# Optimization experiments

Measured on AMD Instinct MI355X. Metric: run time of the kernel, lower is better.

The kernel has to match this reference:

```python
import jax, jax.numpy as jnp
import numpy as np
from jax import lax

DN = ('NCHW', 'OIHW', 'NCHW')


def _conv(x, w, pad):
    return lax.conv_general_dilated(x, w, (1, 1), [(pad, pad), (pad, pad)], dimension_numbers=DN)


def _bn(x, gamma, beta, mean, var, eps=1e-5):
    inv = gamma * lax.rsqrt(var + eps)
    return x * inv[None, :, None, None] + (beta - mean * inv)[None, :, None, None]


def _unfold(x, K, pad):
    # torch.nn.Unfold layout: channel-major, kernel positions fastest -> (B, C, K*K, H, W)
    B, C, H, W = x.shape
    p = lax.conv_general_dilated_patches(x, (K, K), (1, 1), [(pad, pad), (pad, pad)], dimension_numbers=DN)
    return p.reshape(B, C, K * K, H, W)


def setup_inputs() -> dict:
    key = jax.random.key(0)
    ks = jax.random.split(key, 16)
    B, C, H, W, K = 16, 64, 64, 64, 3
    d = {
        'x': jax.random.normal(ks[0], (B, C, H, W), jnp.float32),
        'wq': jax.random.normal(ks[1], (C, C, 1, 1), jnp.float32) * 0.1,
        'wk': jax.random.normal(ks[2], (C, C, K, K), jnp.float32) * 0.05,
        'wv': jax.random.normal(ks[3], (C, C, 1, 1), jnp.float32) * 0.1,
        'pos_h': jax.random.normal(ks[4], (C, K, 1), jnp.float32),
        'pos_w': jax.random.normal(ks[5], (C, 1, K), jnp.float32),
    }
    for i, nm in enumerate(['q', 'k', 'v', 'o']):
        d[nm + '_gamma'] = jnp.ones((C,), jnp.float32)
        d[nm + '_beta'] = jnp.zeros((C,), jnp.float32)
        d[nm + '_mean'] = jax.random.normal(ks[6 + i], (C,), jnp.float32) * 0.1
        d[nm + '_var'] = jax.random.uniform(ks[10 + i], (C,), jnp.float32, 0.5, 1.5)
    return d


def reference(x, wq, q_gamma, q_beta, q_mean, q_var,
              wk, k_gamma, k_beta, k_mean, k_var,
              wv, v_gamma, v_beta, v_mean, v_var,
              pos_h, pos_w, o_gamma, o_beta, o_mean, o_var):
    B, C, H, W = x.shape
    K = pos_h.shape[1]
    heads = C // 8
    cph = C // heads  # channels per head

    q = jax.nn.relu(_bn(_conv(x, wq, 0), q_gamma, q_beta, q_mean, q_var))
    k = jax.nn.relu(_bn(_conv(x, wk, K // 2), k_gamma, k_beta, k_mean, k_var))
    v = _bn(_conv(x, wv, 0), v_gamma, v_beta, v_mean, v_var)

    # local keys + positional bias: (B, C, K*K, H, W)
    unfold_k = _unfold(k, K, K // 2)
    pos = (pos_h + pos_w).reshape(1, C, K * K, 1, 1)
    kp = (unfold_k + pos).reshape(B, heads, cph, K * K, H, W)
    qh = q.reshape(B, heads, cph, 1, H, W)

    attn = (qh * kp).sum(axis=2)            # (B, heads, K*K, H, W)
    attn = jax.nn.softmax(attn, axis=2)

    # local aggregation (LocalConvolution): weights shared across cph channels per head
    uv = _unfold(v, K, (K - 1) // 2).reshape(B, heads, cph, K * K, H, W)
    out = (attn[:, :, None] * uv).sum(axis=3).reshape(B, C, H, W)

    out = jax.nn.relu(_bn(out, o_gamma, o_beta, o_mean, o_var))
    return out
```

## Files before the change

kernel.cpp:

```cpp
#include <hip/hip_runtime.h>
#include <hip/hip_bf16.h>
#include <math.h>

#define B_ 16
#define C_ 64
#define H_ 64
#define W_ 64
#define KSTEPS 18

typedef __attribute__((ext_vector_type(8))) short bf16x8;
typedef __attribute__((ext_vector_type(4))) short bf16x4;
typedef __attribute__((ext_vector_type(4))) float f32x4;

static __device__ __forceinline__ unsigned short f2b(float f) {
    __hip_bfloat16 h = __float2bfloat16(f);
    return *reinterpret_cast<unsigned short*>(&h);
}
static __device__ __forceinline__ float b2f(unsigned short u) {
    __hip_bfloat16 h;
    *reinterpret_cast<unsigned short*>(&h) = u;
    return __bfloat162float(h);
}

__global__ __launch_bounds__(64) void prep_kernel(
    const float* __restrict__ wq, const float* __restrict__ wk, const float* __restrict__ wv,
    const float* __restrict__ qg, const float* __restrict__ qb, const float* __restrict__ qm, const float* __restrict__ qv,
    const float* __restrict__ kg, const float* __restrict__ kb, const float* __restrict__ km, const float* __restrict__ kv,
    const float* __restrict__ vg, const float* __restrict__ vb, const float* __restrict__ vm, const float* __restrict__ vv,
    const float* __restrict__ og, const float* __restrict__ ob, const float* __restrict__ om, const float* __restrict__ ov,
    unsigned short* __restrict__ Wp, float* __restrict__ bnp)
{
    const int bid = blockIdx.x;
    const int lane = threadIdx.x;
    if (bid < 12 * KSTEPS) {
        const int mf = bid / KSTEPS;
        const int ks = bid % KSTEPS;
        const int r = lane & 15;
        bf16x8 u;
#pragma unroll
        for (int j = 0; j < 8; j++) {
            int k = ks * 32 + ((lane >> 4) << 3) + j;
            int tap = k >> 6;
            int c = k & 63;
            float w;
            if (mf < 4)      { int co = mf * 16 + r;        w = (tap == 4) ? wq[co * 64 + c] : 0.f; }
            else if (mf < 8) { int co = (mf - 4) * 16 + r;  w = wk[(co * 64 + c) * 9 + tap]; }
            else             { int co = (mf - 8) * 16 + r;  w = (tap == 4) ? wv[co * 64 + c] : 0.f; }
            u[j] = (short)f2b(w);
        }
        *reinterpret_cast<bf16x8*>(Wp + ((size_t)(mf * KSTEPS + ks) * 64 + lane) * 8) = u;
    } else {
        const int c = lane;
        const float* G[4] = {qg, kg, vg, og};
        const float* Bt[4] = {qb, kb, vb, ob};
        const float* M[4] = {qm, km, vm, om};
        const float* V[4] = {qv, kv, vv, ov};
#pragma unroll
        for (int p = 0; p < 4; p++) {
            float inv = G[p][c] * rsqrtf(V[p][c] + 1e-5f);
            bnp[p * 128 + c] = inv;
            bnp[p * 128 + 64 + c] = Bt[p][c] - M[p][c] * inv;
        }
    }
}

__global__ __launch_bounds__(512) void qkv_mfma2(
    const float* __restrict__ x, const unsigned short* __restrict__ Wp,
    const float* __restrict__ bnp,
    unsigned short* __restrict__ qt, unsigned short* __restrict__ kt, unsigned short* __restrict__ vt)
{
    __shared__ __align__(16) char xs[4 * 66 * 64 * 2];
    __shared__ float bns[384];
    const int bid = blockIdx.x;
    const int b  = bid >> 5;
    const int h0 = (bid & 31) << 1;
    const int tid = threadIdx.x;

    for (int i = tid; i < 4 * 66 * 8; i += 512) {
        int col = i % 66;
        int dy  = (i / 66) & 3;
        int c0g = i / 264;
        int gh = h0 - 1 + dy, gw = col - 1;
        bool ok = ((unsigned)gh < 64u) && ((unsigned)gw < 64u);
        bf16x8 u;
#pragma unroll
        for (int j = 0; j < 8; j++) {
            float f = ok ? x[((b * 64 + c0g * 8 + j) * 64 + gh) * 64 + gw] : 0.f;
            u[j] = (short)f2b(f);
        }
        int La = ((dy * 66 + col) * 64 + c0g * 8) * 2;
        La ^= (col & 7) << 4;
        *reinterpret_cast<bf16x8*>(xs + La) = u;
    }
    if (tid < 384) bns[tid] = bnp[tid];
    __syncthreads();

    const int wid = tid >> 6, lane = tid & 63;
    const int mfg = wid >> 1, nfg = wid & 1;
    const int t = lane & 15, q4 = lane >> 4;

    f32x4 acc[3][4];
#pragma unroll
    for (int m = 0; m < 3; m++)
#pragma unroll
        for (int n = 0; n < 4; n++) acc[m][n] = (f32x4){0.f, 0.f, 0.f, 0.f};

    for (int ks = 0; ks < KSTEPS; ks++) {
        const int tap = ks >> 1;
        const int dy = tap / 3, dx = tap - dy * 3;
        const int kb = (ks & 1) * 32 + q4 * 8;
        bf16x8 bf[4];
#pragma unroll
        for (int n = 0; n < 4; n++) {
            int p = (nfg * 4 + n) * 16 + t;
            int r = p >> 6, colw = p & 63;
            int col = colw + dx;
            int La = (((r + dy) * 66 + col) * 64 + kb) * 2;
            La ^= (col & 7) << 4;
            bf[n] = *reinterpret_cast<const bf16x8*>(xs + La);
        }
#pragma unroll
        for (int m = 0; m < 3; m++) {
            int mf = mfg * 3 + m;
            bf16x8 af = *reinterpret_cast<const bf16x8*>(Wp + ((size_t)(mf * KSTEPS + ks) * 64 + lane) * 8);
#pragma unroll
            for (int n = 0; n < 4; n++)
                acc[m][n] = __builtin_amdgcn_mfma_f32_16x16x32_bf16(af, bf[n], acc[m][n], 0, 0, 0);
        }
    }

#pragma unroll
    for (int m = 0; m < 3; m++) {
        int mf = mfg * 3 + m;
        int plane = mf >> 2;
        int co0 = mf * 16 + q4 * 4;
        int c0 = co0 & 63;
        f32x4 inv  = *reinterpret_cast<const f32x4*>(&bns[plane * 128 + c0]);
        f32x4 bias = *reinterpret_cast<const f32x4*>(&bns[plane * 128 + 64 + c0]);
        unsigned short* base = (plane == 0 ? qt : plane == 1 ? kt : vt);
#pragma unroll
        for (int n = 0; n < 4; n++) {
            int p = (nfg * 4 + n) * 16 + t;
            int r = p >> 6, colw = p & 63;
            bf16x4 pack;
#pragma unroll
            for (int j = 0; j < 4; j++) {
                float val = acc[m][n][j] * inv[j] + bias[j];
                if (plane < 2) val = fmaxf(val, 0.f);
                pack[j] = (short)f2b(val);
            }
            *reinterpret_cast<bf16x4*>(base + ((size_t)((b * 64 + h0 + r) * 64 + colw)) * 64 + c0) = pack;
        }
    }
}

__global__ __launch_bounds__(512) void attn3_kernel(
    const unsigned short* __restrict__ qt, const unsigned short* __restrict__ kt,
    const unsigned short* __restrict__ vt,
    const float* __restrict__ ph, const float* __restrict__ pw,
    const float* __restrict__ bnp, float* __restrict__ out)
{
    __shared__ __align__(16) char ksm[3 * 66 * 64 * 2];
    __shared__ __align__(16) char vsm[3 * 66 * 64 * 2];
    __shared__ float bno[128];
    const int bid = blockIdx.x;
    const int b = bid >> 6;
    const int h = bid & 63;
    const int tid = threadIdx.x;

    for (int i = tid; i < 3 * 66 * 8; i += 512) {
        int c8  = i & 7;
        int pxp = (i >> 3) % 66;
        int dy  = (i >> 3) / 66;
        int gh = h + dy - 1, gw = pxp - 1;
        bool ok = ((unsigned)gh < 64u) && ((unsigned)gw < 64u);
        int La = ((dy * 66 + pxp) * 64 + c8 * 8) * 2;
        La ^= (pxp & 7) << 4;
        bf16x8 kk = (bf16x8){0,0,0,0,0,0,0,0}, vv = kk;
        if (ok) {
            size_t src = ((size_t)((b * 64 + gh) * 64 + gw)) * 64 + c8 * 8;
            kk = *reinterpret_cast<const bf16x8*>(kt + src);
            vv = *reinterpret_cast<const bf16x8*>(vt + src);
        }
        *reinterpret_cast<bf16x8*>(ksm + La) = kk;
        *reinterpret_cast<bf16x8*>(vsm + La) = vv;
    }
    if (tid < 128) bno[tid] = bnp[384 + tid];
    __syncthreads();

    const int px = tid & 63;
    const int head = tid >> 6;
    const int cb = head * 8;

    float qf[8];
    {
        bf16x8 q8 = *reinterpret_cast<const bf16x8*>(qt + ((size_t)((b * 64 + h) * 64 + px)) * 64 + cb);
#pragma unroll
        for (int j = 0; j < 8; j++) qf[j] = b2f((unsigned short)q8[j]);
    }

    float A[3], Bx[3];
#pragma unroll
    for (int tt = 0; tt < 3; tt++) {
        float a = 0.f, bb = 0.f;
#pragma unroll
        for (int j = 0; j < 8; j++) {
            a  = fmaf(qf[j], ph[(cb + j) * 3 + tt], a);
            bb = fmaf(qf[j], pw[(cb + j) * 3 + tt], bb);
        }
        A[tt] = a; Bx[tt] = bb;
    }

    float logit[9];
#pragma unroll
    for (int dy = 0; dy < 3; dy++) {
#pragma unroll
        for (int dx = 0; dx < 3; dx++) {
            int pxp = px + dx;
            int La = ((dy * 66 + pxp) * 64 + cb) * 2;
            La ^= (pxp & 7) << 4;
            bf16x8 k8 = *reinterpret_cast<const bf16x8*>(ksm + La);
            float qk = 0.f;
#pragma unroll
            for (int j = 0; j < 8; j++) qk = fmaf(qf[j], b2f((unsigned short)k8[j]), qk);
            logit[dy * 3 + dx] = qk + A[dy] + Bx[dx];
        }
    }

    float m = logit[0];
#pragma unroll
    for (int tt = 1; tt < 9; tt++) m = fmaxf(m, logit[tt]);
    float e[9], sum = 0.f;
#pragma unroll
    for (int tt = 0; tt < 9; tt++) { e[tt] = __expf(logit[tt] - m); sum += e[tt]; }
    float inv = 1.f / sum;

    float o[8];
#pragma unroll
    for (int j = 0; j < 8; j++) o[j] = 0.f;
#pragma unroll
    for (int dy = 0; dy < 3; dy++) {
#pragma unroll
        for (int dx = 0; dx < 3; dx++) {
            int pxp = px + dx;
            int La = ((dy * 66 + pxp) * 64 + cb) * 2;
            La ^= (pxp & 7) << 4;
            bf16x8 v8 = *reinterpret_cast<const bf16x8*>(vsm + La);
            float w = e[dy * 3 + dx];
#pragma unroll
            for (int j = 0; j < 8; j++) o[j] = fmaf(w, b2f((unsigned short)v8[j]), o[j]);
        }
    }

#pragma unroll
    for (int j = 0; j < 8; j++) {
        int c = cb + j;
        float val = fmaxf(fmaf(o[j] * inv, bno[c], bno[64 + c]), 0.f);
        out[((size_t)(b * C_ + c) * H_ + h) * W_ + px] = val;
    }
}

extern "C" void kernel_launch(void* const* d_in, const int* in_sizes, int n_in,
                              void* d_out, int out_size, void* d_ws, size_t ws_size,
                              hipStream_t stream)
{
    const float* x   = (const float*)d_in[0];
    const float* wq  = (const float*)d_in[1];
    const float* wk  = (const float*)d_in[2];
    const float* wv  = (const float*)d_in[3];
    const float* ph  = (const float*)d_in[4];
    const float* pw  = (const float*)d_in[5];
    const float* qg  = (const float*)d_in[6];
    const float* qb  = (const float*)d_in[7];
    const float* qm  = (const float*)d_in[8];
    const float* qv  = (const float*)d_in[9];
    const float* kg  = (const float*)d_in[10];
    const float* kb  = (const float*)d_in[11];
    const float* km  = (const float*)d_in[12];
    const float* kv  = (const float*)d_in[13];
    const float* vg  = (const float*)d_in[14];
    const float* vb  = (const float*)d_in[15];
    const float* vm  = (const float*)d_in[16];
    const float* vv  = (const float*)d_in[17];
    const float* og  = (const float*)d_in[18];
    const float* ob  = (const float*)d_in[19];
    const float* om  = (const float*)d_in[20];
    const float* ov  = (const float*)d_in[21];

    char* ws = (char*)d_ws;
    unsigned short* Wp = (unsigned short*)ws;
    float* bnp = (float*)(ws + 221184);
    unsigned short* qt = (unsigned short*)(ws + 223232);
    unsigned short* kt = qt + (size_t)B_ * H_ * W_ * C_;
    unsigned short* vt = kt + (size_t)B_ * H_ * W_ * C_;

    prep_kernel<<<12 * KSTEPS + 1, 64, 0, stream>>>(
        wq, wk, wv, qg, qb, qm, qv, kg, kb, km, kv, vg, vb, vm, vv,
        og, ob, om, ov, Wp, bnp);

    qkv_mfma2<<<B_ * H_ / 2, 512, 0, stream>>>(x, Wp, bnp, qt, kt, vt);

    attn3_kernel<<<B_ * H_, 512, 0, stream>>>(qt, kt, vt, ph, pw, bnp, (float*)d_out);
}
```

Measured before the change: 156.3 us.

## Fuse QKV convolution with local attention, recomputing halo rows in shared memory

The QKV MFMA convolution and the attention kernel are merged into one kernel per output row. Each block computes Q, K and V for a 3-row neighborhood (recomputing halo rows that neighbouring blocks also compute) and keeps them in LDS, so the bf16 q/k/v tensors are no longer written to and re-read from global memory. A separate transpose kernel first converts x to a channel-last bf16 layout so the fused kernel can load its 5-row input halo with vector loads. The trade-off is about 1.5x redundant convolution MFMA work, more accumulator registers, and larger LDS use per block.

Result: no change. 157.3 us (+0.6%).

```diff
diff --git a/kernel.cpp b/kernel.cpp
--- a/kernel.cpp
+++ b/kernel.cpp
@@ -64,83 +64,109 @@
     }
 }
 
-__global__ __launch_bounds__(512) void qkv_mfma2(
-    const float* __restrict__ x, const unsigned short* __restrict__ Wp,
+__global__ __launch_bounds__(256) void xt_kernel(
+    const float* __restrict__ x, unsigned short* __restrict__ xt)
+{
+    __shared__ float ls[64][65];
+    const int b = blockIdx.x >> 6;
+    const int h = blockIdx.x & 63;
+    const int tid = threadIdx.x;
+    const int w = tid & 63;
+    const int cg = tid >> 6;
+#pragma unroll
+    for (int cc = 0; cc < 16; cc++) {
+        int c = cg * 16 + cc;
+        ls[c][w] = x[((b * 64 + c) * 64 + h) * 64 + w];
+    }
+    __syncthreads();
+    const int px = tid & 63;
+    bf16x8 u0, u1;
+#pragma unroll
+    for (int j = 0; j < 8; j++) {
+        u0[j] = (short)f2b(ls[cg * 16 + j][px]);
+        u1[j] = (short)f2b(ls[cg * 16 + 8 + j][px]);
+    }
+    size_t base = ((size_t)((b * 64 + h) * 64 + px)) * 64 + cg * 16;
+    *reinterpret_cast<bf16x8*>(xt + base) = u0;
+    *reinterpret_cast<bf16x8*>(xt + base + 8) = u1;
+}
+
+#define KSM_OFF 0
+#define VSM_OFF 25344
+#define QSM_OFF 50688
+__global__ __launch_bounds__(512, 4) void fused_kernel(
+    const unsigned short* __restrict__ xt, const unsigned short* __restrict__ Wp,
     const float* __restrict__ bnp,
-    unsigned short* __restrict__ qt, unsigned short* __restrict__ kt, unsigned short* __restrict__ vt)
+    const float* __restrict__ ph, const float* __restrict__ pw,
+    float* __restrict__ out)
 {
-    __shared__ __align__(16) char xs[4 * 66 * 64 * 2];
-    __shared__ float bns[384];
+    __shared__ __align__(16) char smem[58880];
+    __shared__ float bns[512];
     const int bid = blockIdx.x;
-    const int b  = bid >> 5;
-    const int h0 = (bid & 31) << 1;
+    const int b = bid >> 6;
+    const int h = bid & 63;
     const int tid = threadIdx.x;
 
-    for (int i = tid; i < 4 * 66 * 8; i += 512) {
-        int col = i % 66;
-        int dy  = (i / 66) & 3;
-        int c0g = i / 264;
-        int gh = h0 - 1 + dy, gw = col - 1;
-        bool ok = ((unsigned)gh < 64u) && ((unsigned)gw < 64u);
-        bf16x8 u;
-#pragma unroll
-        for (int j = 0; j < 8; j++) {
-            float f = ok ? x[((b * 64 + c0g * 8 + j) * 64 + gh) * 64 + gw] : 0.f;
-            u[j] = (short)f2b(f);
-        }
-        int La = ((dy * 66 + col) * 64 + c0g * 8) * 2;
+    for (int i = tid; i < 5 * 66 * 8; i += 512) {
+        int ch  = i & 7;
+        int col = (i >> 3) % 66;
+        int dy  = (i >> 3) / 66;
+        int gh = h - 2 + dy, gw = col - 1;
+        bf16x8 u = (bf16x8){0,0,0,0,0,0,0,0};
+        if ((unsigned)gh < 64u && (unsigned)gw < 64u)
+            u = *reinterpret_cast<const bf16x8*>(xt + ((size_t)((b * 64 + gh) * 64 + gw)) * 64 + ch * 8);
+        int La = ((dy * 66 + col) * 64 + ch * 8) * 2;
         La ^= (col & 7) << 4;
-        *reinterpret_cast<bf16x8*>(xs + La) = u;
-    }
-    if (tid < 384) bns[tid] = bnp[tid];
+        *reinterpret_cast<bf16x8*>(smem + La) = u;
+    }
+    bns[tid < 512 ? tid : 0] = bnp[tid < 512 ? tid : 0];
     __syncthreads();
 
     const int wid = tid >> 6, lane = tid & 63;
     const int mfg = wid >> 1, nfg = wid & 1;
     const int t = lane & 15, q4 = lane >> 4;
 
-    f32x4 acc[3][4];
+    f32x4 acc[3][6];
 #pragma unroll
     for (int m = 0; m < 3; m++)
 #pragma unroll
-        for (int n = 0; n < 4; n++) acc[m][n] = (f32x4){0.f, 0.f, 0.f, 0.f};
+        for (int n = 0; n < 6; n++) acc[m][n] = (f32x4){0.f, 0.f, 0.f, 0.f};
 
     for (int ks = 0; ks < KSTEPS; ks++) {
         const int tap = ks >> 1;
         const int dy = tap / 3, dx = tap - dy * 3;
         const int kb = (ks & 1) * 32 + q4 * 8;
-        bf16x8 bf[4];
-#pragma unroll
-        for (int n = 0; n < 4; n++) {
-            int p = (nfg * 4 + n) * 16 + t;
+        bf16x8 bf[6];
+#pragma unroll
+        for (int n = 0; n < 6; n++) {
+            int p = (nfg * 6 + n) * 16 + t;
             int r = p >> 6, colw = p & 63;
             int col = colw + dx;
             int La = (((r + dy) * 66 + col) * 64 + kb) * 2;
             La ^= (col & 7) << 4;
-            bf[n] = *reinterpret_cast<const bf16x8*>(xs + La);
+            bf[n] = *reinterpret_cast<const bf16x8*>(smem + La);
         }
 #pragma unroll
         for (int m = 0; m < 3; m++) {
             int mf = mfg * 3 + m;
             bf16x8 af = *reinterpret_cast<const bf16x8*>(Wp + ((size_t)(mf * KSTEPS + ks) * 64 + lane) * 8);
 #pragma unroll
-            for (int n = 0; n < 4; n++)
+            for (int n = 0; n < 6; n++)
                 acc[m][n] = __builtin_amdgcn_mfma_f32_16x16x32_bf16(af, bf[n], acc[m][n], 0, 0, 0);
         }
     }
+    __syncthreads();
 
 #pragma unroll
     for (int m = 0; m < 3; m++) {
         int mf = mfg * 3 + m;
         int plane = mf >> 2;
-        int co0 = mf * 16 + q4 * 4;
-        int c0 = co0 & 63;
+        int c0 = (mf * 16 + q4 * 4) & 63;
         f32x4 inv  = *reinterpret_cast<const f32x4*>(&bns[plane * 128 + c0]);
         f32x4 bias = *reinterpret_cast<const f32x4*>(&bns[plane * 128 + 64 + c0]);
-        unsigned short* base = (plane == 0 ? qt : plane == 1 ? kt : vt);
-#pragma unroll
-        for (int n = 0; n < 4; n++) {
-            int p = (nfg * 4 + n) * 16 + t;
+#pragma unroll
+        for (int n = 0; n < 6; n++) {
+            int p = (nfg * 6 + n) * 16 + t;
             int r = p >> 6, colw = p & 63;
             bf16x4 pack;
 #pragma unroll
@@ -149,43 +175,46 @@
                 if (plane < 2) val = fmaxf(val, 0.f);
                 pack[j] = (short)f2b(val);
             }
-            *reinterpret_cast<bf16x4*>(base + ((size_t)((b * 64 + h0 + r) * 64 + colw)) * 64 + c0) = pack;
-        }
-    }
-}
-
-__global__ __launch_bounds__(512) void attn3_kernel(
-    const unsigned short* __restrict__ qt, const unsigned short* __restrict__ kt,
-    const unsigned short* __restrict__ vt,
-    const float* __restrict__ ph, const float* __restrict__ pw,
-    const float* __restrict__ bnp, float* __restrict__ out)
-{
-    __shared__ __align__(16) char ksm[3 * 66 * 64 * 2];
-    __shared__ __align__(16) char vsm[3 * 66 * 64 * 2];
-    __shared__ float bno[128];
-    const int bid = blockIdx.x;
-    const int b = bid >> 6;
-    const int h = bid & 63;
-    const int tid = threadIdx.x;
-
-    for (int i = tid; i < 3 * 66 * 8; i += 512) {
-        int c8  = i & 7;
-        int pxp = (i >> 3) % 66;
-        int dy  = (i >> 3) / 66;
-        int gh = h + dy - 1, gw = pxp - 1;
-        bool ok = ((unsigned)gh < 64u) && ((unsigned)gw < 64u);
-        int La = ((dy * 66 + pxp) * 64 + c8 * 8) * 2;
-        La ^= (pxp & 7) << 4;
-        bf16x8 kk = (bf16x8){0,0,0,0,0,0,0,0}, vv = kk;
-        if (ok) {
-            size_t src = ((size_t)((b * 64 + gh) * 64 + gw)) * 64 + c8 * 8;
-            kk = *reinterpret_cast<const bf16x8*>(kt + src);
-            vv = *reinterpret_cast<const bf16x8*>(vt + src);
-        }
-        *reinterpret_cast<bf16x8*>(ksm + La) = kk;
-        *reinterpret_cast<bf16x8*>(vsm + La) = vv;
-    }
-    if (tid < 128) bno[tid] = bnp[384 + tid];
+            if (plane == 0) {
+                if (r == 1) {
+                    int La = (colw * 64 + c0) * 2;
+                    La ^= (colw & 7) << 4;
+                    *reinterpret_cast<bf16x4*>(smem + QSM_OFF + La) = pack;
+                }
+            } else {
+                int pxp = colw + 1;
+                int La = ((r * 66 + pxp) * 64 + c0) * 2;
+                La ^= (pxp & 7) << 4;
+                *reinterpret_cast<bf16x4*>(smem + (plane == 1 ? KSM_OFF : VSM_OFF) + La) = pack;
+            }
+        }
+    }
+    __syncthreads();
+
+    const bf16x8 z8 = (bf16x8){0,0,0,0,0,0,0,0};
+    for (int i = tid; i < 96; i += 512) {
+        int buf = i & 1;
+        int j = i >> 1;
+        int ch = j & 7;
+        int jj = j >> 3;
+        int col = (jj & 1) ? 65 : 0;
+        int rr = jj >> 1;
+        int La = ((rr * 66 + col) * 64 + ch * 8) * 2;
+        La ^= (col & 7) << 4;
+        *reinterpret_cast<bf16x8*>(smem + (buf ? VSM_OFF : KSM_OFF) + La) = z8;
+    }
+    int rbad = (h == 0) ? 0 : ((h == 63) ? 2 : -1);
+    if (rbad >= 0) {
+        for (int i = tid; i < 66 * 8 * 2; i += 512) {
+            int buf = i & 1;
+            int j = i >> 1;
+            int ch = j & 7;
+            int col = j >> 3;
+            int La = ((rbad * 66 + col) * 64 + ch * 8) * 2;
+            La ^= (col & 7) << 4;
+            *reinterpret_cast<bf16x8*>(smem + (buf ? VSM_OFF : KSM_OFF) + La) = z8;
+        }
+    }
     __syncthreads();
 
     const int px = tid & 63;
@@ -194,7 +223,9 @@
 
     float qf[8];
     {
-        bf16x8 q8 = *reinterpret_cast<const bf16x8*>(qt + ((size_t)((b * 64 + h) * 64 + px)) * 64 + cb);
+        int Lq = (px * 64 + cb) * 2;
+        Lq ^= (px & 7) << 4;
+        bf16x8 q8 = *reinterpret_cast<const bf16x8*>(smem + QSM_OFF + Lq);
 #pragma unroll
         for (int j = 0; j < 8; j++) qf[j] = b2f((unsigned short)q8[j]);
     }
@@ -219,7 +250,7 @@
             int pxp = px + dx;
             int La = ((dy * 66 + pxp) * 64 + cb) * 2;
             La ^= (pxp & 7) << 4;
-            bf16x8 k8 = *reinterpret_cast<const bf16x8*>(ksm + La);
+            bf16x8 k8 = *reinterpret_cast<const bf16x8*>(smem + KSM_OFF + La);
             float qk = 0.f;
 #pragma unroll
             for (int j = 0; j < 8; j++) qk = fmaf(qf[j], b2f((unsigned short)k8[j]), qk);
@@ -227,12 +258,12 @@
         }
     }
 
-    float m = logit[0];
-#pragma unroll
-    for (int tt = 1; tt < 9; tt++) m = fmaxf(m, logit[tt]);
+    float mx = logit[0];
+#pragma unroll
+    for (int tt = 1; tt < 9; tt++) mx = fmaxf(mx, logit[tt]);
     float e[9], sum = 0.f;
 #pragma unroll
-    for (int tt = 0; tt < 9; tt++) { e[tt] = __expf(logit[tt] - m); sum += e[tt]; }
+    for (int tt = 0; tt < 9; tt++) { e[tt] = __expf(logit[tt] - mx); sum += e[tt]; }
     float inv = 1.f / sum;
 
     float o[8];
@@ -245,7 +276,7 @@
             int pxp = px + dx;
             int La = ((dy * 66 + pxp) * 64 + cb) * 2;
             La ^= (pxp & 7) << 4;
-            bf16x8 v8 = *reinterpret_cast<const bf16x8*>(vsm + La);
+            bf16x8 v8 = *reinterpret_cast<const bf16x8*>(smem + VSM_OFF + La);
             float w = e[dy * 3 + dx];
 #pragma unroll
             for (int j = 0; j < 8; j++) o[j] = fmaf(w, b2f((unsigned short)v8[j]), o[j]);
@@ -255,7 +286,7 @@
 #pragma unroll
     for (int j = 0; j < 8; j++) {
         int c = cb + j;
-        float val = fmaxf(fmaf(o[j] * inv, bno[c], bno[64 + c]), 0.f);
+        float val = fmaxf(fmaf(o[j] * inv, bns[384 + c], bns[384 + 64 + c]), 0.f);
         out[((size_t)(b * C_ + c) * H_ + h) * W_ + px] = val;
     }
 }
@@ -290,15 +321,13 @@
     char* ws = (char*)d_ws;
     unsigned short* Wp = (unsigned short*)ws;
     float* bnp = (float*)(ws + 221184);
-    unsigned short* qt = (unsigned short*)(ws + 223232);
-    unsigned short* kt = qt + (size_t)B_ * H_ * W_ * C_;
-    unsigned short* vt = kt + (size_t)B_ * H_ * W_ * C_;
+    unsigned short* xt = (unsigned short*)(ws + 223232);
 
     prep_kernel<<<12 * KSTEPS + 1, 64, 0, stream>>>(
         wq, wk, wv, qg, qb, qm, qv, kg, kb, km, kv, vg, vb, vm, vv,
         og, ob, om, ov, Wp, bnp);
 
-    qkv_mfma2<<<B_ * H_ / 2, 512, 0, stream>>>(x, Wp, bnp, qt, kt, vt);
-
-    attn3_kernel<<<B_ * H_, 512, 0, stream>>>(qt, kt, vt, ph, pw, bnp, (float*)d_out);
-}
+    xt_kernel<<<B_ * H_, 256, 0, stream>>>(x, xt);
+
+    fused_kernel<<<B_ * H_, 512, 0, stream>>>(xt, Wp, bnp, ph, pw, (float*)d_out);
+}
```
